# Kernel tuning notes

Measured on AMD Instinct MI355X. Metric: run time of the kernel, lower is better.

The kernel has to match this reference:

```python
import jax, jax.numpy as jnp
import numpy as np

CHUNK = 64  # rows of A processed per step; bounds the [CHUNK,K,N] intermediate


def setup_inputs() -> dict:
    key = jax.random.key(0)
    k1, k2, k3 = jax.random.split(key, 3)
    in_features, out_features = 768, 768
    x = jax.random.normal(k1, (2, 1024, in_features), dtype=jnp.float32)
    # kaiming_uniform_(a=sqrt(5)) on [out,in] -> bound = 1/sqrt(in_features)
    wb = 1.0 / np.sqrt(in_features)
    weight = jax.random.uniform(k2, (out_features, in_features), minval=-wb, maxval=wb, dtype=jnp.float32)
    bias = jax.random.uniform(k3, (out_features,), minval=-wb, maxval=wb, dtype=jnp.float32)
    return {"x": x, "weight": weight, "bias": bias}


def _mam(A, B):
    # A: [M, K], B: [K, N]. C[i,j] = max_k A[i,k]*B[k,j] + min_k A[i,k]*B[k,j]
    M, K = A.shape
    N = B.shape[1]
    def chunk_fn(a):  # a: [CHUNK, K]
        p = a[:, :, None] * B[None, :, :]  # [CHUNK, K, N]
        return jnp.max(p, axis=1) + jnp.min(p, axis=1)
    n_chunks = M // CHUNK
    C = jax.lax.map(chunk_fn, A.reshape(n_chunks, CHUNK, K))  # [n_chunks, CHUNK, N]
    return C.reshape(M, N)


def reference(x, weight, bias):
    # beta = 0 path: pure MAM + bias (matches MAMDense.forward with beta=False)
    K = x.shape[-1]
    x_flat = x.reshape(-1, K)               # [M, K]
    C = _mam(x_flat, weight.T)              # [M, N]
    C = C + bias[None, :]
    return C.reshape(x.shape[:-1] + (weight.shape[0],))
```

## Files before the change

kernel.cpp:

```cpp
#include <hip/hip_runtime.h>
#include <math.h>


#define M_DIM 2048
#define N_DIM 768
#define K_DIM 768

#define BM 64
#define BN 32
#define BK 64
#define KP (BK / 2)
#define NTILES (K_DIM / BK)

#define SAH 66
#define SBH 34

typedef _Float16 h2 __attribute__((ext_vector_type(2)));
typedef _Float16 h4 __attribute__((ext_vector_type(4)));

__device__ __forceinline__ h2 cvt_pk(float x, float y) {
    return __builtin_bit_cast(h2, __builtin_amdgcn_cvt_pkrtz(x, y));
}

__global__ __launch_bounds__(256, 3) void mam_kernel(
    const float* __restrict__ A, const float* __restrict__ W,
    const float* __restrict__ bias, float* __restrict__ out)
{
    __shared__ __align__(16) h2 As[KP * SAH];
    __shared__ __align__(16) h2 Bs[KP * SBH];

    const int tid = threadIdx.x;
    const int m0 = blockIdx.y * BM;
    const int n0 = blockIdx.x * BN;
    const int mt = tid >> 4;
    const int nt = tid & 15;

    h2 pmax[4][2], pmin[4][2];
    const _Float16 HMIN = (_Float16)(-65504.0f), HMAX = (_Float16)(65504.0f);
#pragma unroll
    for (int i = 0; i < 4; ++i)
#pragma unroll
        for (int j = 0; j < 2; ++j) {
            pmax[i][j] = (h2){HMIN, HMIN};
            pmin[i][j] = (h2){HMAX, HMAX};
        }

    const int arow = tid >> 4;
    const int akc  = tid & 15;
    const float* Ap = A + (size_t)m0 * K_DIM + akc * 4;
    const float* Wp = W + (size_t)n0 * K_DIM + akc * 4;

    const float bb0 = bias[n0 + nt * 2 + 0];
    const float bb1 = bias[n0 + nt * 2 + 1];

    h2* awr = &As[2 * akc * SAH];
    h2* bwr = &Bs[2 * akc * SBH];
    const h2* Ard = &As[mt * 4];
    const h2* Brd = &Bs[nt * 2];

    float4 pa[4], pb[2];
#pragma unroll
    for (int q = 0; q < 4; ++q)
        pa[q] = *(const float4*)(Ap + (size_t)(arow + 16 * q) * K_DIM);
#pragma unroll
    for (int q = 0; q < 2; ++q)
        pb[q] = *(const float4*)(Wp + (size_t)(arow + 16 * q) * K_DIM);

    for (int kt = 0; kt < NTILES; ++kt) {
        if (kt) __syncthreads();

#pragma unroll
        for (int q = 0; q < 4; ++q) {
            awr[0 * SAH + arow + 16 * q] = cvt_pk(pa[q].x, pa[q].y);
            awr[1 * SAH + arow + 16 * q] = cvt_pk(pa[q].z, pa[q].w);
        }
#pragma unroll
        for (int q = 0; q < 2; ++q) {
            bwr[0 * SBH + arow + 16 * q] = cvt_pk(pb[q].x, pb[q].y);
            bwr[1 * SBH + arow + 16 * q] = cvt_pk(pb[q].z, pb[q].w);
        }
        __syncthreads();

        if (kt + 1 < NTILES) {
            const float* An = Ap + (kt + 1) * BK;
            const float* Wn = Wp + (kt + 1) * BK;
#pragma unroll
            for (int q = 0; q < 4; ++q)
                pa[q] = *(const float4*)(An + (size_t)(arow + 16 * q) * K_DIM);
#pragma unroll
            for (int q = 0; q < 2; ++q)
                pb[q] = *(const float4*)(Wn + (size_t)(arow + 16 * q) * K_DIM);
        }

#pragma unroll
        for (int kk2 = 0; kk2 < KP; ++kk2) {
            const h4 a01 = *(const h4*)(Ard + kk2 * SAH);
            const h4 a23 = *(const h4*)(Ard + kk2 * SAH + 2);
            const h4 b01 = *(const h4*)(Brd + kk2 * SBH);
            const h2 am[4] = {a01.xy, a01.zw, a23.xy, a23.zw};
            const h2 bn[2] = {b01.xy, b01.zw};
#pragma unroll
            for (int i = 0; i < 4; ++i)
#pragma unroll
                for (int j = 0; j < 2; ++j) {
                    const h2 p = am[i] * bn[j];
                    pmax[i][j] = __builtin_elementwise_max(pmax[i][j], p);
                    pmin[i][j] = __builtin_elementwise_min(pmin[i][j], p);
                }
        }
    }

#pragma unroll
    for (int i = 0; i < 4; ++i) {
        float2 o;
        o.x = fmaxf((float)pmax[i][0].x, (float)pmax[i][0].y)
            + fminf((float)pmin[i][0].x, (float)pmin[i][0].y) + bb0;
        o.y = fmaxf((float)pmax[i][1].x, (float)pmax[i][1].y)
            + fminf((float)pmin[i][1].x, (float)pmin[i][1].y) + bb1;
        *(float2*)&out[(size_t)(m0 + mt * 4 + i) * N_DIM + n0 + nt * 2] = o;
    }
}

extern "C" void kernel_launch(void* const* d_in, const int* in_sizes, int n_in,
                              void* d_out, int out_size, void* d_ws, size_t ws_size,
                              hipStream_t stream) {
    const float* x    = (const float*)d_in[0];
    const float* w    = (const float*)d_in[1];
    const float* bias = (const float*)d_in[2];
    float* out = (float*)d_out;

    dim3 grid(N_DIM / BN, M_DIM / BM);
    mam_kernel<<<grid, 256, 0, stream>>>(x, w, bias, out);
}
```

Measured before the change: 68.85 us.

## Double-buffer shared-memory tiles and widen A reads to 16-byte loads

Shared tiles for A and B become double-buffered, so each tile iteration needs one barrier instead of two. The next tile's shared-memory write overlaps with computation on the current buffer. The A row stride is padded to 68 half2 so each thread can read its four A values with a single 16-byte LDS load instead of two 8-byte loads. This doubles LDS use per block, which could limit occupancy, and the main loop is manually unrolled by two.

```diff
diff --git a/kernel.cpp b/kernel.cpp
--- a/kernel.cpp
+++ b/kernel.cpp
@@ -12,11 +12,12 @@
 #define KP (BK / 2)
 #define NTILES (K_DIM / BK)
 
-#define SAH 66
+#define SAH 68
 #define SBH 34
 
 typedef _Float16 h2 __attribute__((ext_vector_type(2)));
 typedef _Float16 h4 __attribute__((ext_vector_type(4)));
+typedef _Float16 h8 __attribute__((ext_vector_type(8)));
 
 __device__ __forceinline__ h2 cvt_pk(float x, float y) {
     return __builtin_bit_cast(h2, __builtin_amdgcn_cvt_pkrtz(x, y));
@@ -26,8 +27,8 @@
     const float* __restrict__ A, const float* __restrict__ W,
     const float* __restrict__ bias, float* __restrict__ out)
 {
-    __shared__ __align__(16) h2 As[KP * SAH];
-    __shared__ __align__(16) h2 Bs[KP * SBH];
+    __shared__ __align__(16) h2 As[2][KP * SAH];
+    __shared__ __align__(16) h2 Bs[2][KP * SBH];
 
     const int tid = threadIdx.x;
     const int m0 = blockIdx.y * BM;
@@ -47,68 +48,87 @@
 
     const int arow = tid >> 4;
     const int akc  = tid & 15;
-    const float* Ap = A + (size_t)m0 * K_DIM + akc * 4;
-    const float* Wp = W + (size_t)n0 * K_DIM + akc * 4;
+    const float* Ap = A + (size_t)(m0 + arow) * K_DIM + akc * 4;
+    const float* Wp = W + (size_t)(n0 + arow) * K_DIM + akc * 4;
 
     const float bb0 = bias[n0 + nt * 2 + 0];
     const float bb1 = bias[n0 + nt * 2 + 1];
 
-    h2* awr = &As[2 * akc * SAH];
-    h2* bwr = &Bs[2 * akc * SBH];
-    const h2* Ard = &As[mt * 4];
-    const h2* Brd = &Bs[nt * 2];
+    float4 pa0, pa1, pa2, pa3, pb0, pb1;
 
-    float4 pa[4], pb[2];
-#pragma unroll
-    for (int q = 0; q < 4; ++q)
-        pa[q] = *(const float4*)(Ap + (size_t)(arow + 16 * q) * K_DIM);
-#pragma unroll
-    for (int q = 0; q < 2; ++q)
-        pb[q] = *(const float4*)(Wp + (size_t)(arow + 16 * q) * K_DIM);
+#define GLOAD(t) do {                                                        \
+        const float* An_ = Ap + (t) * BK;                                    \
+        const float* Wn_ = Wp + (t) * BK;                                    \
+        pa0 = *(const float4*)(An_ + (size_t)( 0) * K_DIM);                  \
+        pa1 = *(const float4*)(An_ + (size_t)(16) * K_DIM);                  \
+        pa2 = *(const float4*)(An_ + (size_t)(32) * K_DIM);                  \
+        pa3 = *(const float4*)(An_ + (size_t)(48) * K_DIM);                  \
+        pb0 = *(const float4*)(Wn_ + (size_t)( 0) * K_DIM);                  \
+        pb1 = *(const float4*)(Wn_ + (size_t)(16) * K_DIM);                  \
+    } while (0)
 
-    for (int kt = 0; kt < NTILES; ++kt) {
-        if (kt) __syncthreads();
+#define SWRITE(buf) do {                                                     \
+        h2* Aw_ = &As[buf][2 * akc * SAH + arow];                            \
+        Aw_[0]            = cvt_pk(pa0.x, pa0.y);                            \
+        Aw_[SAH]          = cvt_pk(pa0.z, pa0.w);                            \
+        Aw_[16]           = cvt_pk(pa1.x, pa1.y);                            \
+        Aw_[SAH + 16]     = cvt_pk(pa1.z, pa1.w);                            \
+        Aw_[32]           = cvt_pk(pa2.x, pa2.y);                            \
+        Aw_[SAH + 32]     = cvt_pk(pa2.z, pa2.w);                            \
+        Aw_[48]           = cvt_pk(pa3.x, pa3.y);                            \
+        Aw_[SAH + 48]     = cvt_pk(pa3.z, pa3.w);                            \
+        h2* Bw_ = &Bs[buf][2 * akc * SBH + arow];                            \
+        Bw_[0]            = cvt_pk(pb0.x, pb0.y);                            \
+        Bw_[SBH]          = cvt_pk(pb0.z, pb0.w);                            \
+        Bw_[16]           = cvt_pk(pb1.x, pb1.y);                            \
+        Bw_[SBH + 16]     = cvt_pk(pb1.z, pb1.w);                            \
+    } while (0)
 
-#pragma unroll
-        for (int q = 0; q < 4; ++q) {
-            awr[0 * SAH + arow + 16 * q] = cvt_pk(pa[q].x, pa[q].y);
-            awr[1 * SAH + arow + 16 * q] = cvt_pk(pa[q].z, pa[q].w);
-        }
-#pragma unroll
-        for (int q = 0; q < 2; ++q) {
-            bwr[0 * SBH + arow + 16 * q] = cvt_pk(pb[q].x, pb[q].y);
-            bwr[1 * SBH + arow + 16 * q] = cvt_pk(pb[q].z, pb[q].w);
-        }
+#define COMPUTE(buf) do {                                                    \
+        const h2* Ab_ = &As[buf][mt * 4];                                    \
+        const h2* Bb_ = &Bs[buf][nt * 2];                                    \
+        _Pragma("unroll")                                                    \
+        for (int kk2 = 0; kk2 < KP; ++kk2) {                                 \
+            const h8 a_ = *(const h8*)(Ab_ + kk2 * SAH);                     \
+            const h4 b_ = *(const h4*)(Bb_ + kk2 * SBH);                     \
+            const h2 am0 = __builtin_shufflevector(a_, a_, 0, 1);            \
+            const h2 am1 = __builtin_shufflevector(a_, a_, 2, 3);            \
+            const h2 am2 = __builtin_shufflevector(a_, a_, 4, 5);            \
+            const h2 am3 = __builtin_shufflevector(a_, a_, 6, 7);            \
+            const h2 bn0 = __builtin_shufflevector(b_, b_, 0, 1);            \
+            const h2 bn1 = __builtin_shufflevector(b_, b_, 2, 3);            \
+            h2 p_;                                                           \
+            p_ = am0 * bn0; pmax[0][0] = __builtin_elementwise_max(pmax[0][0], p_); pmin[0][0] = __builtin_elementwise_min(pmin[0][0], p_); \
+            p_ = am0 * bn1; pmax[0][1] = __builtin_elementwise_max(pmax[0][1], p_); pmin[0][1] = __builtin_elementwise_min(pmin[0][1], p_); \
+            p_ = am1 * bn0; pmax[1][0] = __builtin_elementwise_max(pmax[1][0], p_); pmin[1][0] = __builtin_elementwise_min(pmin[1][0], p_); \
+            p_ = am1 * bn1; pmax[1][1] = __builtin_elementwise_max(pmax[1][1], p_); pmin[1][1] = __builtin_elementwise_min(pmin[1][1], p_); \
+            p_ = am2 * bn0; pmax[2][0] = __builtin_elementwise_max(pmax[2][0], p_); pmin[2][0] = __builtin_elementwise_min(pmin[2][0], p_); \
+            p_ = am2 * bn1; pmax[2][1] = __builtin_elementwise_max(pmax[2][1], p_); pmin[2][1] = __builtin_elementwise_min(pmin[2][1], p_); \
+            p_ = am3 * bn0; pmax[3][0] = __builtin_elementwise_max(pmax[3][0], p_); pmin[3][0] = __builtin_elementwise_min(pmin[3][0], p_); \
+            p_ = am3 * bn1; pmax[3][1] = __builtin_elementwise_max(pmax[3][1], p_); pmin[3][1] = __builtin_elementwise_min(pmin[3][1], p_); \
+        }                                                                    \
+    } while (0)
+
+    GLOAD(0);
+    SWRITE(0);
+    __syncthreads();
+
+#pragma unroll 1
+    for (int ktt = 0; ktt < NTILES / 2 - 1; ++ktt) {
+        GLOAD(2 * ktt + 1);
+        COMPUTE(0);
+        SWRITE(1);
         __syncthreads();
-
-        if (kt + 1 < NTILES) {
-            const float* An = Ap + (kt + 1) * BK;
-            const float* Wn = Wp + (kt + 1) * BK;
-#pragma unroll
-            for (int q = 0; q < 4; ++q)
-                pa[q] = *(const float4*)(An + (size_t)(arow + 16 * q) * K_DIM);
-#pragma unroll
-            for (int q = 0; q < 2; ++q)
-                pb[q] = *(const float4*)(Wn + (size_t)(arow + 16 * q) * K_DIM);
-        }
-
-#pragma unroll
-        for (int kk2 = 0; kk2 < KP; ++kk2) {
-            const h4 a01 = *(const h4*)(Ard + kk2 * SAH);
-            const h4 a23 = *(const h4*)(Ard + kk2 * SAH + 2);
-            const h4 b01 = *(const h4*)(Brd + kk2 * SBH);
-            const h2 am[4] = {a01.xy, a01.zw, a23.xy, a23.zw};
-            const h2 bn[2] = {b01.xy, b01.zw};
-#pragma unroll
-            for (int i = 0; i < 4; ++i)
-#pragma unroll
-                for (int j = 0; j < 2; ++j) {
-                    const h2 p = am[i] * bn[j];
-                    pmax[i][j] = __builtin_elementwise_max(pmax[i][j], p);
-                    pmin[i][j] = __builtin_elementwise_min(pmin[i][j], p);
-                }
-        }
+        GLOAD(2 * ktt + 2);
+        COMPUTE(1);
+        SWRITE(0);
+        __syncthreads();
     }
+    GLOAD(NTILES - 1);
+    COMPUTE(0);
+    SWRITE(1);
+    __syncthreads();
+    COMPUTE(1);
 
 #pragma unroll
     for (int i = 0; i < 4; ++i) {
```

Result: no change. 69.29 us (+0.6%).
